# Performance work log

Measured on AMD Instinct MI355X. Metric: run time of the kernel, lower is better.

The kernel has to match this reference:

```python
import jax, jax.numpy as jnp
import numpy as np

N_NODES = 50000
N_EDGES = 800000
D_NODE = 64
D_EDGE = 64
MSG_DIM = 64           # n_features_list_messages[-1]
MLP_FEATS = [128, 128, 64]  # n_features_list_nodes
LN_EPS = 1e-6


def setup_inputs() -> dict:
    key = jax.random.key(0)
    ks = jax.random.split(key, 16)
    nodes = jax.random.normal(ks[0], (N_NODES, D_NODE), dtype=jnp.float32)
    edges = jax.random.normal(ks[1], (N_EDGES, D_EDGE), dtype=jnp.float32)
    senders = jax.random.randint(ks[2], (N_EDGES,), 0, N_NODES, dtype=jnp.int32)
    receivers = jax.random.randint(ks[3], (N_EDGES,), 0, N_NODES, dtype=jnp.int32)

    def glorot(k, shape):
        fan_in, fan_out = shape[0], shape[1]
        s = jnp.sqrt(2.0 / (fan_in + fan_out))
        return jax.random.normal(k, shape, dtype=jnp.float32) * s

    W_message = glorot(ks[4], (D_NODE + D_EDGE, MSG_DIM))      # no bias
    W_node = glorot(ks[5], (D_NODE, MLP_FEATS[-1]))            # no bias
    mlp_in_dim = D_NODE + MSG_DIM
    mlp_w0 = glorot(ks[6], (mlp_in_dim, MLP_FEATS[0]))
    mlp_b0 = jnp.zeros((MLP_FEATS[0],), dtype=jnp.float32)
    mlp_w1 = glorot(ks[7], (MLP_FEATS[0], MLP_FEATS[1]))
    mlp_b1 = jnp.zeros((MLP_FEATS[1],), dtype=jnp.float32)
    mlp_w2 = glorot(ks[8], (MLP_FEATS[1], MLP_FEATS[2]))
    mlp_b2 = jnp.zeros((MLP_FEATS[2],), dtype=jnp.float32)
    ln_scale = jnp.ones((MLP_FEATS[-1],), dtype=jnp.float32)
    ln_bias = jnp.zeros((MLP_FEATS[-1],), dtype=jnp.float32)

    return {
        "nodes": nodes, "edges": edges, "senders": senders, "receivers": receivers,
        "W_message": W_message, "W_node": W_node,
        "mlp_w0": mlp_w0, "mlp_b0": mlp_b0,
        "mlp_w1": mlp_w1, "mlp_b1": mlp_b1,
        "mlp_w2": mlp_w2, "mlp_b2": mlp_b2,
        "ln_scale": ln_scale, "ln_bias": ln_bias,
    }


def reference(nodes, edges, senders, receivers, W_message, W_node,
              mlp_w0, mlp_b0, mlp_w1, mlp_b1, mlp_w2, mlp_b2,
              ln_scale, ln_bias):
    # gather sender node features [E, d_node]
    sender_features = nodes[senders]
    # linear message on concat(sender, edge) [E, msg_dim]
    msg_in = jnp.concatenate([sender_features, edges], axis=-1)
    messages = msg_in @ W_message
    # scatter-add into receiver buckets [N, msg_dim]
    aggregated = jax.ops.segment_sum(messages, receivers, num_segments=N_NODES)
    # node MLP with ReLU hidden layers, linear output
    h = jnp.concatenate([nodes, aggregated], axis=-1)
    h = jax.nn.relu(h @ mlp_w0 + mlp_b0)
    h = jax.nn.relu(h @ mlp_w1 + mlp_b1)
    nodes_out = h @ mlp_w2 + mlp_b2
    # residual (linear skip) + LayerNorm
    x = nodes @ W_node + nodes_out
    mu = jnp.mean(x, axis=-1, keepdims=True)
    var = jnp.var(x, axis=-1, keepdims=True)
    nodes_new = (x - mu) * jax.lax.rsqrt(var + LN_EPS) * ln_scale + ln_bias
    return nodes_new
```

## Files before the change

kernel.cpp:

```cpp
#include <hip/hip_runtime.h>
#include <cstdint>
#include <cstddef>


__global__ void hist_k(const int* __restrict__ recv, int* __restrict__ hist, int E){
  int i = blockIdx.x*blockDim.x + threadIdx.x;
  if (i < E) atomicAdd(&hist[recv[i]], 1);
}

__global__ void s1_k(const int* __restrict__ hist, int* __restrict__ partial, int Nn){
  __shared__ int sh[256];
  int t = threadIdx.x;
  int i = blockIdx.x*256 + t;
  sh[t] = (i < Nn) ? hist[i] : 0;
  __syncthreads();
  for (int off = 128; off > 0; off >>= 1){
    if (t < off) sh[t] += sh[t + off];
    __syncthreads();
  }
  if (t == 0) partial[blockIdx.x] = sh[0];
}

__global__ void s2_k(int* __restrict__ partial, int nb){
  if (blockIdx.x == 0 && threadIdx.x == 0){
    int run = 0;
    for (int b = 0; b < nb; b++){ int v = partial[b]; partial[b] = run; run += v; }
  }
}

__global__ void s3_k(const int* __restrict__ hist, const int* __restrict__ partial,
                     int* __restrict__ offsets, int* __restrict__ cursor, int Nn){
  __shared__ int sh[256];
  int t = threadIdx.x;
  int i = blockIdx.x*256 + t;
  int v = (i < Nn) ? hist[i] : 0;
  sh[t] = v;
  __syncthreads();
  for (int off = 1; off < 256; off <<= 1){
    int x = (t >= off) ? sh[t - off] : 0;
    __syncthreads();
    sh[t] += x;
    __syncthreads();
  }
  if (i < Nn){
    int excl = sh[t] - v + partial[blockIdx.x];
    offsets[i] = excl;
    cursor[i]  = excl;
  }
}

__global__ void fill_k(const int* __restrict__ recv, int* __restrict__ cursor,
                       int* __restrict__ csr, int E){
  int i = blockIdx.x*blockDim.x + threadIdx.x;
  if (i < E){
    int r = recv[i];
    int pos = atomicAdd(&cursor[r], 1);
    csr[pos] = i;
  }
}

__global__ __launch_bounds__(256) void gather_sum_k(
    const float* __restrict__ nodes, const float* __restrict__ edges,
    const int* __restrict__ senders, const int* __restrict__ offsets,
    const int* __restrict__ hist, const int* __restrict__ csr,
    float* __restrict__ SE, int Nn)
{
  int wid  = threadIdx.x >> 6;
  int lane = threadIdx.x & 63;
  int node = blockIdx.x*4 + wid;
  if (node >= Nn) return;
  int start = offsets[node];
  int cnt   = hist[node];
  float sa = 0.f, ea = 0.f;
  int i = 0;
  for (; i + 2 <= cnt; i += 2){
    int e0 = csr[start + i], e1 = csr[start + i + 1];
    int s0 = senders[e0],    s1 = senders[e1];
    float n0 = nodes[(size_t)s0*64 + lane];
    float n1 = nodes[(size_t)s1*64 + lane];
    float g0 = edges[(size_t)e0*64 + lane];
    float g1 = edges[(size_t)e1*64 + lane];
    sa += n0 + n1;
    ea += g0 + g1;
  }
  if (i < cnt){
    int e0 = csr[start + i];
    int s0 = senders[e0];
    sa += nodes[(size_t)s0*64 + lane];
    ea += edges[(size_t)e0*64 + lane];
  }
  SE[(size_t)node*128 + lane]      = sa;
  SE[(size_t)node*128 + 64 + lane] = ea;
}

__global__ void transpose_k(const float* __restrict__ in, float* __restrict__ out, int R, int C){
  __shared__ float tile[32][33];
  int c0 = blockIdx.x*32, r0 = blockIdx.y*32;
  int tx = threadIdx.x, ty = threadIdx.y;
  #pragma unroll
  for (int i = 0; i < 32; i += 8){
    int r = r0 + ty + i, c = c0 + tx;
    if (r < R && c < C) tile[ty + i][tx] = in[(size_t)r*C + c];
  }
  __syncthreads();
  #pragma unroll
  for (int i = 0; i < 32; i += 8){
    int c = c0 + ty + i, r = r0 + tx;
    if (r < R && c < C) out[(size_t)c*R + r] = tile[tx][ty + i];
  }
}

__global__ void wprep_k(const float* __restrict__ Wmsg, const float* __restrict__ w0,
                        const float* __restrict__ w2, const float* __restrict__ Wnode,
                        float* __restrict__ W1eff, float* __restrict__ W3eff){
  int idx = blockIdx.x*blockDim.x + threadIdx.x;
  if (idx < 192*128){
    int r = idx >> 7, j = idx & 127;
    float v;
    if (r < 64) v = w0[r*128 + j];
    else {
      int kk = r - 64;
      float a = 0.f;
      for (int m = 0; m < 64; m++) a = fmaf(Wmsg[kk*64 + m], w0[(64 + m)*128 + j], a);
      v = a;
    }
    W1eff[idx] = v;
  }
  if (idx < 192*64){
    int r = idx >> 6, j = idx & 63;
    W3eff[idx] = (r < 128) ? w2[r*64 + j] : Wnode[(r - 128)*64 + j];
  }
}


__global__ __launch_bounds__(256) void layer1_k(
    const float* __restrict__ nodesT, const float* __restrict__ SET,
    const float* __restrict__ W, const float* __restrict__ bias,
    float* __restrict__ outT, int N)
{
  int n  = blockIdx.x*256 + threadIdx.x;
  int jb = blockIdx.y*32;
  if (n >= N) return;
  float acc[32];
  #pragma unroll
  for (int j = 0; j < 32; j++) acc[j] = bias[jb + j];
  for (int k = 0; k < 64; k++){
    float x = nodesT[(size_t)k*N + n];
    #pragma unroll
    for (int j = 0; j < 32; j++) acc[j] = fmaf(x, W[k*128 + jb + j], acc[j]);
  }
  for (int k = 0; k < 128; k++){
    float x = SET[(size_t)k*N + n];
    #pragma unroll
    for (int j = 0; j < 32; j++) acc[j] = fmaf(x, W[(64 + k)*128 + jb + j], acc[j]);
  }
  #pragma unroll
  for (int j = 0; j < 32; j++) outT[(size_t)(jb + j)*N + n] = fmaxf(acc[j], 0.f);
}

__global__ __launch_bounds__(256) void layer2_k(
    const float* __restrict__ inT, const float* __restrict__ W, const float* __restrict__ bias,
    float* __restrict__ outT, int N)
{
  int n  = blockIdx.x*256 + threadIdx.x;
  int jb = blockIdx.y*32;
  if (n >= N) return;
  float acc[32];
  #pragma unroll
  for (int j = 0; j < 32; j++) acc[j] = bias[jb + j];
  for (int k = 0; k < 128; k++){
    float x = inT[(size_t)k*N + n];
    #pragma unroll
    for (int j = 0; j < 32; j++) acc[j] = fmaf(x, W[k*128 + jb + j], acc[j]);
  }
  #pragma unroll
  for (int j = 0; j < 32; j++) outT[(size_t)(jb + j)*N + n] = fmaxf(acc[j], 0.f);
}

__global__ __launch_bounds__(256) void layer3_k(
    const float* __restrict__ X2T, const float* __restrict__ nodesT,
    const float* __restrict__ W, const float* __restrict__ bias,
    const float* __restrict__ ln_scale, const float* __restrict__ ln_bias,
    float* __restrict__ out, int N)
{
  int n = blockIdx.x*256 + threadIdx.x;
  if (n >= N) return;
  float acc[64];
  #pragma unroll
  for (int j = 0; j < 64; j++) acc[j] = bias[j];
  for (int k = 0; k < 128; k++){
    float x = X2T[(size_t)k*N + n];
    #pragma unroll
    for (int j = 0; j < 64; j++) acc[j] = fmaf(x, W[k*64 + j], acc[j]);
  }
  for (int k = 0; k < 64; k++){
    float x = nodesT[(size_t)k*N + n];
    #pragma unroll
    for (int j = 0; j < 64; j++) acc[j] = fmaf(x, W[(128 + k)*64 + j], acc[j]);
  }
  float mu = 0.f;
  #pragma unroll
  for (int j = 0; j < 64; j++) mu += acc[j];
  mu *= (1.f/64.f);
  float var = 0.f;
  #pragma unroll
  for (int j = 0; j < 64; j++){ float d = acc[j] - mu; var = fmaf(d, d, var); }
  var *= (1.f/64.f);
  float inv = rsqrtf(var + 1e-6f);
  float4* o = (float4*)(out + (size_t)n*64);
  #pragma unroll
  for (int q = 0; q < 16; q++){
    float y0 = (acc[4*q+0] - mu)*inv*ln_scale[4*q+0] + ln_bias[4*q+0];
    float y1 = (acc[4*q+1] - mu)*inv*ln_scale[4*q+1] + ln_bias[4*q+1];
    float y2 = (acc[4*q+2] - mu)*inv*ln_scale[4*q+2] + ln_bias[4*q+2];
    float y3 = (acc[4*q+3] - mu)*inv*ln_scale[4*q+3] + ln_bias[4*q+3];
    o[q] = make_float4(y0, y1, y2, y3);
  }
}


extern "C" void kernel_launch(void* const* d_in, const int* in_sizes, int n_in,
                              void* d_out, int out_size, void* d_ws, size_t ws_size,
                              hipStream_t stream)
{
  const float* nodes   = (const float*)d_in[0];
  const float* edges   = (const float*)d_in[1];
  const int*   senders = (const int*)d_in[2];
  const int*   recv    = (const int*)d_in[3];
  const float* Wmsg    = (const float*)d_in[4];
  const float* Wnode   = (const float*)d_in[5];
  const float* w0      = (const float*)d_in[6];
  const float* b0      = (const float*)d_in[7];
  const float* w1      = (const float*)d_in[8];
  const float* b1      = (const float*)d_in[9];
  const float* w2      = (const float*)d_in[10];
  const float* b2      = (const float*)d_in[11];
  const float* lns     = (const float*)d_in[12];
  const float* lnb     = (const float*)d_in[13];
  float* out = (float*)d_out;

  const int N = in_sizes[0] / 64;
  const int E = in_sizes[2];

  auto align256 = [](size_t x){ return (x + 255) & ~(size_t)255; };
  char* p = (char*)d_ws;
  int* hist    = (int*)p; p += align256((size_t)N*4);
  int* offsets = (int*)p; p += align256((size_t)N*4);
  int* cursor  = (int*)p; p += align256((size_t)N*4);
  int* partial = (int*)p; p += align256(1024);
  int* csr     = (int*)p; p += align256((size_t)E*4);
  float* W1eff = (float*)p; p += align256((size_t)192*128*4);
  float* W3eff = (float*)p; p += align256((size_t)192*64*4);
  float* nodesT= (float*)p; p += align256((size_t)64*N*4);
  float* bufA  = (float*)p; p += align256((size_t)128*N*4);
  float* bufB  = (float*)p; p += align256((size_t)128*N*4);

  hipMemsetAsync(hist, 0, (size_t)N*4, stream);

  const int gridE = (E + 255)/256;
  const int nb    = (N + 255)/256;

  hist_k<<<gridE, 256, 0, stream>>>(recv, hist, E);
  s1_k<<<nb, 256, 0, stream>>>(hist, partial, N);
  s2_k<<<1, 64, 0, stream>>>(partial, nb);
  s3_k<<<nb, 256, 0, stream>>>(hist, partial, offsets, cursor, N);
  fill_k<<<gridE, 256, 0, stream>>>(recv, cursor, csr, E);

  gather_sum_k<<<(N + 3)/4, 256, 0, stream>>>(nodes, edges, senders, offsets, hist, csr, bufA, N);

  dim3 tb(32, 8);
  transpose_k<<<dim3(2, (N + 31)/32), tb, 0, stream>>>(nodes, nodesT, N, 64);
  transpose_k<<<dim3(4, (N + 31)/32), tb, 0, stream>>>(bufA, bufB, N, 128);

  wprep_k<<<(192*128 + 255)/256, 256, 0, stream>>>(Wmsg, w0, w2, Wnode, W1eff, W3eff);

  layer1_k<<<dim3(nb, 4), 256, 0, stream>>>(nodesT, bufB, W1eff, b0, bufA, N);
  layer2_k<<<dim3(nb, 4), 256, 0, stream>>>(bufA, w1, b1, bufB, N);
  layer3_k<<<nb, 256, 0, stream>>>(bufB, nodesT, W3eff, b2, lns, lnb, out, N);
}
```

Baseline: 695.7 us.

## Pack sender ids into CSR, batch-load edge ids via shuffles, widen MLP tiles

The fill kernel now stores (edge id, sender id) pairs, so the gather kernel no longer does a dependent load from senders. The gather loads up to 64 packed entries per wave in one coalesced read and broadcasts them with shuffles, unrolled by 4 to keep more loads in flight. The serial single-thread block scan becomes a wave-level shuffle scan. The layer1 and layer2 kernels compute 64 outputs per thread instead of 32, halving redundant input reads at the cost of higher register pressure.

```diff
diff --git a/kernel.cpp b/kernel.cpp
--- a/kernel.cpp
+++ b/kernel.cpp
@@ -22,9 +22,18 @@
 }
 
 __global__ void s2_k(int* __restrict__ partial, int nb){
-  if (blockIdx.x == 0 && threadIdx.x == 0){
-    int run = 0;
-    for (int b = 0; b < nb; b++){ int v = partial[b]; partial[b] = run; run += v; }
+  int lane = threadIdx.x;
+  int run = 0;
+  for (int base = 0; base < nb; base += 64){
+    int v = (base + lane < nb) ? partial[base + lane] : 0;
+    int x = v;
+    #pragma unroll
+    for (int off = 1; off < 64; off <<= 1){
+      int y = __shfl_up(x, off);
+      if (lane >= off) x += y;
+    }
+    if (base + lane < nb) partial[base + lane] = x - v + run;
+    run += __shfl(x, 63);
   }
 }
 
@@ -49,21 +58,21 @@
   }
 }
 
-__global__ void fill_k(const int* __restrict__ recv, int* __restrict__ cursor,
-                       int* __restrict__ csr, int E){
+__global__ void fill_k(const int* __restrict__ recv, const int* __restrict__ senders,
+                       int* __restrict__ cursor, int2* __restrict__ csr_pack, int E){
   int i = blockIdx.x*blockDim.x + threadIdx.x;
   if (i < E){
     int r = recv[i];
+    int s = senders[i];
     int pos = atomicAdd(&cursor[r], 1);
-    csr[pos] = i;
+    csr_pack[pos] = make_int2(i, s);
   }
 }
 
 __global__ __launch_bounds__(256) void gather_sum_k(
     const float* __restrict__ nodes, const float* __restrict__ edges,
-    const int* __restrict__ senders, const int* __restrict__ offsets,
-    const int* __restrict__ hist, const int* __restrict__ csr,
-    float* __restrict__ SE, int Nn)
+    const int2* __restrict__ csr_pack, const int* __restrict__ offsets,
+    const int* __restrict__ hist, float* __restrict__ SE, int Nn)
 {
   int wid  = threadIdx.x >> 6;
   int lane = threadIdx.x & 63;
@@ -72,22 +81,34 @@
   int start = offsets[node];
   int cnt   = hist[node];
   float sa = 0.f, ea = 0.f;
-  int i = 0;
-  for (; i + 2 <= cnt; i += 2){
-    int e0 = csr[start + i], e1 = csr[start + i + 1];
-    int s0 = senders[e0],    s1 = senders[e1];
-    float n0 = nodes[(size_t)s0*64 + lane];
-    float n1 = nodes[(size_t)s1*64 + lane];
-    float g0 = edges[(size_t)e0*64 + lane];
-    float g1 = edges[(size_t)e1*64 + lane];
-    sa += n0 + n1;
-    ea += g0 + g1;
-  }
-  if (i < cnt){
-    int e0 = csr[start + i];
-    int s0 = senders[e0];
-    sa += nodes[(size_t)s0*64 + lane];
-    ea += edges[(size_t)e0*64 + lane];
+  int done = 0;
+  while (done < cnt){
+    int m = cnt - done; if (m > 64) m = 64;
+    int2 pk = make_int2(0, 0);
+    if (lane < m) pk = csr_pack[start + done + lane];
+    int u = 0;
+    for (; u + 4 <= m; u += 4){
+      int e0 = __shfl(pk.x, u+0), s0 = __shfl(pk.y, u+0);
+      int e1 = __shfl(pk.x, u+1), s1 = __shfl(pk.y, u+1);
+      int e2 = __shfl(pk.x, u+2), s2 = __shfl(pk.y, u+2);
+      int e3 = __shfl(pk.x, u+3), s3 = __shfl(pk.y, u+3);
+      float n0 = nodes[(size_t)s0*64 + lane];
+      float n1 = nodes[(size_t)s1*64 + lane];
+      float n2 = nodes[(size_t)s2*64 + lane];
+      float n3 = nodes[(size_t)s3*64 + lane];
+      float g0 = edges[(size_t)e0*64 + lane];
+      float g1 = edges[(size_t)e1*64 + lane];
+      float g2 = edges[(size_t)e2*64 + lane];
+      float g3 = edges[(size_t)e3*64 + lane];
+      sa += (n0 + n1) + (n2 + n3);
+      ea += (g0 + g1) + (g2 + g3);
+    }
+    for (; u < m; u++){
+      int e0 = __shfl(pk.x, u), s0 = __shfl(pk.y, u);
+      sa += nodes[(size_t)s0*64 + lane];
+      ea += edges[(size_t)e0*64 + lane];
+    }
+    done += m;
   }
   SE[(size_t)node*128 + lane]      = sa;
   SE[(size_t)node*128 + 64 + lane] = ea;
@@ -139,23 +160,23 @@
     float* __restrict__ outT, int N)
 {
   int n  = blockIdx.x*256 + threadIdx.x;
-  int jb = blockIdx.y*32;
+  int jb = blockIdx.y*64;
   if (n >= N) return;
-  float acc[32];
-  #pragma unroll
-  for (int j = 0; j < 32; j++) acc[j] = bias[jb + j];
+  float acc[64];
+  #pragma unroll
+  for (int j = 0; j < 64; j++) acc[j] = bias[jb + j];
   for (int k = 0; k < 64; k++){
     float x = nodesT[(size_t)k*N + n];
     #pragma unroll
-    for (int j = 0; j < 32; j++) acc[j] = fmaf(x, W[k*128 + jb + j], acc[j]);
+    for (int j = 0; j < 64; j++) acc[j] = fmaf(x, W[k*128 + jb + j], acc[j]);
   }
   for (int k = 0; k < 128; k++){
     float x = SET[(size_t)k*N + n];
     #pragma unroll
-    for (int j = 0; j < 32; j++) acc[j] = fmaf(x, W[(64 + k)*128 + jb + j], acc[j]);
-  }
-  #pragma unroll
-  for (int j = 0; j < 32; j++) outT[(size_t)(jb + j)*N + n] = fmaxf(acc[j], 0.f);
+    for (int j = 0; j < 64; j++) acc[j] = fmaf(x, W[(64 + k)*128 + jb + j], acc[j]);
+  }
+  #pragma unroll
+  for (int j = 0; j < 64; j++) outT[(size_t)(jb + j)*N + n] = fmaxf(acc[j], 0.f);
 }
 
 __global__ __launch_bounds__(256) void layer2_k(
@@ -163,18 +184,18 @@
     float* __restrict__ outT, int N)
 {
   int n  = blockIdx.x*256 + threadIdx.x;
-  int jb = blockIdx.y*32;
+  int jb = blockIdx.y*64;
   if (n >= N) return;
-  float acc[32];
-  #pragma unroll
-  for (int j = 0; j < 32; j++) acc[j] = bias[jb + j];
+  float acc[64];
+  #pragma unroll
+  for (int j = 0; j < 64; j++) acc[j] = bias[jb + j];
   for (int k = 0; k < 128; k++){
     float x = inT[(size_t)k*N + n];
     #pragma unroll
-    for (int j = 0; j < 32; j++) acc[j] = fmaf(x, W[k*128 + jb + j], acc[j]);
-  }
-  #pragma unroll
-  for (int j = 0; j < 32; j++) outT[(size_t)(jb + j)*N + n] = fmaxf(acc[j], 0.f);
+    for (int j = 0; j < 64; j++) acc[j] = fmaf(x, W[k*128 + jb + j], acc[j]);
+  }
+  #pragma unroll
+  for (int j = 0; j < 64; j++) outT[(size_t)(jb + j)*N + n] = fmaxf(acc[j], 0.f);
 }
 
 __global__ __launch_bounds__(256) void layer3_k(
@@ -248,7 +269,7 @@
   int* offsets = (int*)p; p += align256((size_t)N*4);
   int* cursor  = (int*)p; p += align256((size_t)N*4);
   int* partial = (int*)p; p += align256(1024);
-  int* csr     = (int*)p; p += align256((size_t)E*4);
+  int2* csr_pack = (int2*)p; p += align256((size_t)E*8);
   float* W1eff = (float*)p; p += align256((size_t)192*128*4);
   float* W3eff = (float*)p; p += align256((size_t)192*64*4);
   float* nodesT= (float*)p; p += align256((size_t)64*N*4);
@@ -264,9 +285,9 @@
   s1_k<<<nb, 256, 0, stream>>>(hist, partial, N);
   s2_k<<<1, 64, 0, stream>>>(partial, nb);
   s3_k<<<nb, 256, 0, stream>>>(hist, partial, offsets, cursor, N);
-  fill_k<<<gridE, 256, 0, stream>>>(recv, cursor, csr, E);
-
-  gather_sum_k<<<(N + 3)/4, 256, 0, stream>>>(nodes, edges, senders, offsets, hist, csr, bufA, N);
+  fill_k<<<gridE, 256, 0, stream>>>(recv, senders, cursor, csr_pack, E);
+
+  gather_sum_k<<<(N + 3)/4, 256, 0, stream>>>(nodes, edges, csr_pack, offsets, hist, bufA, N);
 
   dim3 tb(32, 8);
   transpose_k<<<dim3(2, (N + 31)/32), tb, 0, stream>>>(nodes, nodesT, N, 64);
@@ -274,7 +295,7 @@
 
   wprep_k<<<(192*128 + 255)/256, 256, 0, stream>>>(Wmsg, w0, w2, Wnode, W1eff, W3eff);
 
-  layer1_k<<<dim3(nb, 4), 256, 0, stream>>>(nodesT, bufB, W1eff, b0, bufA, N);
-  layer2_k<<<dim3(nb, 4), 256, 0, stream>>>(bufA, w1, b1, bufB, N);
+  layer1_k<<<dim3(nb, 2), 256, 0, stream>>>(nodesT, bufB, W1eff, b0, bufA, N);
+  layer2_k<<<dim3(nb, 2), 256, 0, stream>>>(bufA, w1, b1, bufB, N);
   layer3_k<<<nb, 256, 0, stream>>>(bufB, nodesT, W3eff, b2, lns, lnb, out, N);
 }
```

New measurement: 644.4 us. -7.4%, faster.
